# Kernel tuning notes

Hardware: AMD Instinct MI355X
Metric: run time of the kernel (lower is better)

The kernel has to match this reference:

```python
import jax, jax.numpy as jnp
import numpy as np

IOU_TH = 0.5      # iou_threshold
SCORE_TH = 0.5    # confidence_threshold (passed as score_threshold to tf NMS)
MAX_DET = 512     # max_detections


def setup_inputs() -> dict:
    key = jax.random.key(0)
    k1, k2, k3 = jax.random.split(key, 3)
    B, N, C = 8, 2048, 80
    # tf.image.non_max_suppression interprets box columns as corners
    # (y1, x1, y2, x2); generate valid corner boxes in [0, 1].
    mins = jax.random.uniform(k1, (B, N, 2), dtype=jnp.float32)
    sizes = jax.random.uniform(k2, (B, N, 2), dtype=jnp.float32) * 0.2 + 0.01
    box_prediction = jnp.concatenate([mins, mins + sizes], axis=-1)  # [B,N,4]
    class_prediction = jax.random.normal(k3, (B, N, C), dtype=jnp.float32) * 2.0
    return {"box_prediction": box_prediction, "class_prediction": class_prediction}


def _nms_single(boxes, cls_pred, conf):
    """Greedy NMS for one image. boxes [N,4], cls_pred [N,C], conf [N].
    Matches tf.image.non_max_suppression semantics (corner-coordinate IoU,
    score threshold, greedy suppression in descending score order),
    then gathers boxes/cls/conf at the kept indices, padded to MAX_DET."""
    N = boxes.shape[0]
    order = jnp.argsort(-conf)                 # descending scores
    b = boxes[order]                            # [N,4]
    c = cls_pred[order]                         # [N,C]
    s = conf[order]                             # [N]

    bb = jax.lax.stop_gradient(b)               # IoU/indices are non-diff
    y1, x1, y2, x2 = bb[:, 0], bb[:, 1], bb[:, 2], bb[:, 3]
    area = (y2 - y1) * (x2 - x1)                # [N]
    ih = jnp.clip(jnp.minimum(y2[:, None], y2[None, :]) -
                  jnp.maximum(y1[:, None], y1[None, :]), 0.0)
    iw = jnp.clip(jnp.minimum(x2[:, None], x2[None, :]) -
                  jnp.maximum(x1[:, None], x1[None, :]), 0.0)
    inter = ih * iw                             # [N,N]
    union = area[:, None] + area[None, :] - inter
    iou = inter / jnp.maximum(union, 1e-9)      # [N,N]

    valid = s > SCORE_TH                        # score_threshold filter
    idxs = jnp.arange(N)

    def step(keep, xs):
        row, i = xs
        # if box i survives, suppress all later boxes overlapping > IOU_TH
        sup = (row > IOU_TH) & (idxs > i) & keep[i]
        return keep & ~sup, None

    keep, _ = jax.lax.scan(step, valid, (iou, idxs))

    # select kept boxes (already sorted by score) padded to MAX_DET
    masked = jnp.where(keep, s, -1.0)
    top_s, top_idx = jax.lax.top_k(jax.lax.stop_gradient(masked), MAX_DET)
    vm = top_s > SCORE_TH                       # validity of each output slot
    out_box = b[top_idx] * vm[:, None].astype(b.dtype)
    out_cls = c[top_idx] * vm[:, None].astype(c.dtype)
    out_conf = jnp.where(vm, s[top_idx], 0.0)
    return out_box, out_cls, out_conf


def reference(box_prediction, class_prediction):
    # from_logits=True branch of the layer
    class_confidence = jnp.max(jax.nn.sigmoid(class_prediction), axis=-1)  # [B,N]
    cls_prob = jax.nn.softmax(class_prediction, axis=-1)                   # [B,N,C]
    nms_box, nms_cls, nms_conf = jax.vmap(_nms_single)(
        box_prediction, cls_prob, class_confidence)
    return nms_box, nms_cls, nms_conf
```

## Files before the change

### kernel.cpp

```cpp
#include <hip/hip_runtime.h>
#include <stdint.h>

#define BB 8
#define NN 2048
#define NC 80
#define MAXDET 512
#define WPR 32


#define ORD_HALF 0xBF000000u

__global__ void k_conf(const float* __restrict__ cls, uint64_t* __restrict__ keys) {
    int gid = blockIdx.x * blockDim.x + threadIdx.x;
    const float4* p = (const float4*)(cls + (size_t)gid * NC);
    float m = -3.0e38f;
#pragma unroll
    for (int i = 0; i < NC / 4; ++i) {
        float4 v = p[i];
        m = fmaxf(m, fmaxf(fmaxf(v.x, v.y), fmaxf(v.z, v.w)));
    }
    float e  = expf(-m);
    float cf = 1.0f / (1.0f + e);
    uint32_t u = __float_as_uint(cf);
    u = (u & 0x80000000u) ? ~u : (u | 0x80000000u);
    int n = gid & (NN - 1);
    keys[gid] = ((uint64_t)u << 32) | (uint32_t)(NN - 1 - n);
}

#define RCHUNK 128
__global__ __launch_bounds__(512) void k_rank(const uint64_t* __restrict__ keys_in,
                                              uint64_t* __restrict__ keys_out,
                                              const float* __restrict__ boxes,
                                              float* __restrict__ sboxes) {
    __shared__ uint64_t sk[NN];
    __shared__ uint16_t part[4][RCHUNK];
    int b = blockIdx.y, t = threadIdx.x;
    const uint64_t* kin = keys_in + (size_t)b * NN;
#pragma unroll
    for (int j = 0; j < NN / 512; ++j)
        sk[t + j * 512] = kin[t + j * 512];
    __syncthreads();
    int sub = t >> 7;
    int el  = t & (RCHUNK - 1);
    int e   = blockIdx.x * RCHUNK + el;
    uint64_t mykey = sk[e];
    int base = sub * (NN / 4);
    int r = 0;
    for (int mm = 0; mm < NN / 4; ++mm)
        r += (sk[base + mm] > mykey) ? 1 : 0;
    part[sub][el] = (uint16_t)r;
    __syncthreads();
    if (t < RCHUNK) {
        int rank = part[0][t] + part[1][t] + part[2][t] + part[3][t];
        keys_out[(size_t)b * NN + rank] = mykey;
        int orig = (NN - 1) - (int)(mykey & 0xFFFFFFFFull);
        ((float4*)sboxes)[(size_t)b * NN + rank] =
            ((const float4*)boxes)[(size_t)b * NN + orig];
    }
}

__global__ void k_sup(const float* __restrict__ sboxes, uint64_t* __restrict__ sup) {
#pragma clang fp contract(off)
    __shared__ float cy1[256], cx1[256], cy2[256], cx2[256], car[256];
    __shared__ float ry1[64], rx1[64], ry2[64], rx2[64], rar[64];
    int rt = blockIdx.x, ct = blockIdx.y, b = blockIdx.z;
    int t = threadIdx.x;
    int col0 = ct << 8, row0 = rt << 6;
    {
        float4 bx = ((const float4*)sboxes)[(size_t)b * NN + col0 + t];
        cy1[t] = bx.x; cx1[t] = bx.y; cy2[t] = bx.z; cx2[t] = bx.w;
        car[t] = (bx.z - bx.x) * (bx.w - bx.y);
        if (t < 64) {
            float4 rb = ((const float4*)sboxes)[(size_t)b * NN + row0 + t];
            ry1[t] = rb.x; rx1[t] = rb.y; ry2[t] = rb.z; rx2[t] = rb.w;
            rar[t] = (rb.z - rb.x) * (rb.w - rb.y);
        }
    }
    __syncthreads();
    int lr = t & 63, lg = t >> 6;
    int r = row0 + lr;
    int gw = (ct << 2) + lg;
    int cbase = gw << 6;
    uint64_t w = 0;
    if (cbase + 63 > r) {
        float y1 = ry1[lr], x1 = rx1[lr], y2 = ry2[lr], x2 = rx2[lr], ar = rar[lr];
        int lcb = lg << 6;
        for (int c = 0; c < 64; ++c) {
            int lc = lcb + c;
            float ih = fmaxf(fminf(y2, cy2[lc]) - fmaxf(y1, cy1[lc]), 0.0f);
            float iw = fmaxf(fminf(x2, cx2[lc]) - fmaxf(x1, cx1[lc]), 0.0f);
            float inter = ih * iw;
            float uni = (ar + car[lc]) - inter;
            float iou = inter / fmaxf(uni, 1e-9f);
            if ((iou > 0.5f) & ((cbase + c) > r)) w |= (1ull << c);
        }
    }
    sup[((size_t)b * NN + r) * WPR + gw] = w;
}

#define NMS_THREADS 320
__global__ __launch_bounds__(NMS_THREADS) void k_nms(const uint64_t* __restrict__ keys,
                                                     const float* __restrict__ sboxes,
                                                     const uint64_t* __restrict__ sup,
                                                     int* __restrict__ kidx,
                                                     int* __restrict__ kcount,
                                                     float* __restrict__ out_box,
                                                     float* __restrict__ out_conf) {
    __shared__ uint64_t buf[2][64 * WPR];
    __shared__ uint8_t  val[NN];
    __shared__ uint64_t kmaskS[WPR];
    __shared__ int pfx[WPR];
    __shared__ int s_kc;
    __shared__ int s_done;
    int b = blockIdx.x, t = threadIdx.x;
    const uint64_t* supb = sup + (size_t)b * NN * WPR;
    const uint64_t* keyb = keys + (size_t)b * NN;

    for (int i = t; i < NN; i += NMS_THREADS)
        val[i] = (uint8_t)((uint32_t)(keyb[i] >> 32) > ORD_HALF);
    if (t < WPR) kmaskS[t] = 0;
    if (t == 0) s_done = 0;
    for (int w = t; w < 64 * WPR / 2; w += NMS_THREADS)
        ((float4*)buf[0])[w] = ((const float4*)supb)[w];
    __syncthreads();

    int wave = t >> 6;
    uint64_t kb = 0;
    int cnt = 0;
    if (t < 32) {
        uint64_t vm = 0;
#pragma unroll
        for (int c = 0; c < 64; ++c)
            vm |= ((uint64_t)val[(t << 6) | c]) << c;
        kb = ~vm;
    }
    int l2 = t & 31, half = (t >> 5) & 1;

    for (int g = 0; g < WPR; ++g) {
        if (wave > 0) {
            if (g + 1 < WPR) {
                const float4* src = (const float4*)(supb + (size_t)(g + 1) * 64 * WPR);
                float4* dst = (float4*)buf[(g + 1) & 1];
                int idx = t - 64;
                float4 r0 = src[idx];
                float4 r1 = src[idx + 256];
                float4 r2 = src[idx + 512];
                float4 r3 = src[idx + 768];
                dst[idx]       = r0;
                dst[idx + 256] = r1;
                dst[idx + 512] = r2;
                dst[idx + 768] = r3;
            }
        } else {
            const uint64_t* bufc = buf[g & 1];
            uint64_t diag = bufc[t * WPR + g];
            uint32_t dlo = (uint32_t)diag, dhi = (uint32_t)(diag >> 32);
            uint64_t rwv = __shfl(kb, g);
            uint32_t rw_lo = __builtin_amdgcn_readfirstlane((uint32_t)rwv);
            uint32_t rw_hi = __builtin_amdgcn_readfirstlane((uint32_t)(rwv >> 32));
            uint32_t gm_lo = 0, gm_hi = 0;
#pragma unroll
            for (int c = 0; c < 32; ++c) {
                uint32_t rlo = __builtin_amdgcn_readlane(dlo, c);
                uint32_t rhi = __builtin_amdgcn_readlane(dhi, c);
                if (((rw_lo >> c) & 1u) == 0u) {
                    rw_lo |= rlo; rw_hi |= rhi; gm_lo |= (1u << c);
                }
            }
#pragma unroll
            for (int c = 0; c < 32; ++c) {
                uint32_t rlo = __builtin_amdgcn_readlane(dlo, c + 32);
                uint32_t rhi = __builtin_amdgcn_readlane(dhi, c + 32);
                if (((rw_hi >> c) & 1u) == 0u) {
                    rw_lo |= rlo; rw_hi |= rhi; gm_hi |= (1u << c);
                }
            }
            uint64_t gm = ((uint64_t)gm_hi << 32) | gm_lo;
            uint32_t gmh = half ? gm_hi : gm_lo;
            const uint64_t* rowp = bufc + ((half << 5) * WPR + l2);
            uint64_t acc = 0;
#pragma unroll
            for (int j = 0; j < 32; ++j) {
                uint64_t row = rowp[(size_t)j * WPR];
                if ((gmh >> j) & 1u) acc |= row;
            }
            acc |= __shfl(acc, t ^ 32);
            if (t < 32) kb |= acc;
            if (t == g) kmaskS[g] = gm;
            cnt += __popcll(gm);
            if (cnt >= MAXDET) s_done = 1;
        }
        __syncthreads();
        if (s_done) break;
    }

    if (t == 0) {
        int s = 0;
        for (int w2 = 0; w2 < WPR; ++w2) { pfx[w2] = s; s += __popcll(kmaskS[w2]); }
        s_kc = (s < MAXDET) ? s : MAXDET;
        kcount[b] = s_kc;
    }
    __syncthreads();
    for (int i = t; i < NN; i += NMS_THREADS) {
        uint64_t m = kmaskS[i >> 6];
        if ((m >> (i & 63)) & 1ull) {
            int rank = pfx[i >> 6] + __popcll(m & ((1ull << (i & 63)) - 1ull));
            if (rank < MAXDET) {
                ((float4*)out_box)[(size_t)b * MAXDET + rank] =
                    ((const float4*)sboxes)[(size_t)b * NN + i];
                uint64_t kk = keyb[i];
                uint32_t u = (uint32_t)(kk >> 32);
                float cf = (u & 0x80000000u) ? __uint_as_float(u ^ 0x80000000u)
                                             : __uint_as_float(~u);
                out_conf[(size_t)b * MAXDET + rank] = cf;
                kidx[b * MAXDET + rank] = (NN - 1) - (int)(kk & 0xFFFFFFFFull);
            }
        }
    }
    for (int k = s_kc + t; k < MAXDET; k += NMS_THREADS) {
        ((float4*)out_box)[(size_t)b * MAXDET + k] = make_float4(0.f, 0.f, 0.f, 0.f);
        out_conf[(size_t)b * MAXDET + k] = 0.0f;
    }
}

__global__ void k_softmax(const float* __restrict__ cls, const int* __restrict__ kidx,
                          const int* __restrict__ kcount, float* __restrict__ out_cls) {
    int k = blockIdx.x, b = blockIdx.y, lane = threadIdx.x;
    float* dst = out_cls + ((size_t)b * MAXDET + k) * NC;
    if (k >= kcount[b]) {
        dst[lane] = 0.0f;
        if (lane < NC - 64) dst[64 + lane] = 0.0f;
        return;
    }
    int n = kidx[b * MAXDET + k];
    const float* src = cls + ((size_t)b * NN + n) * NC;
    float x0 = src[lane];
    float x1 = (lane < NC - 64) ? src[64 + lane] : -3.0e38f;
    float m = fmaxf(x0, x1);
    for (int o = 32; o > 0; o >>= 1) m = fmaxf(m, __shfl_xor(m, o));
    float e0 = expf(x0 - m);
    float e1 = (lane < NC - 64) ? expf(x1 - m) : 0.0f;
    float s = e0 + e1;
    for (int o = 32; o > 0; o >>= 1) s += __shfl_xor(s, o);
    dst[lane] = e0 / s;
    if (lane < NC - 64) dst[64 + lane] = e1 / s;
}

extern "C" void kernel_launch(void* const* d_in, const int* in_sizes, int n_in,
                              void* d_out, int out_size, void* d_ws, size_t ws_size,
                              hipStream_t stream) {
    const float* boxes = (const float*)d_in[0];
    const float* cls   = (const float*)d_in[1];
    float* out      = (float*)d_out;
    float* out_box  = out;
    float* out_cls  = out + BB * MAXDET * 4;
    float* out_conf = out + BB * MAXDET * (4 + NC);

    char* ws = (char*)d_ws;
    uint64_t* keysA  = (uint64_t*)(ws + 0);
    uint64_t* keysB  = (uint64_t*)(ws + 131072);
    float*    sboxes = (float*)(ws + 262144);
    int*      kidx   = (int*)(ws + 524288);
    int*      kcount = (int*)(ws + 540672);
    uint64_t* sup    = (uint64_t*)(ws + 544768);

    k_conf<<<(BB * NN) / 256, 256, 0, stream>>>(cls, keysA);
    k_rank<<<dim3(NN / RCHUNK, BB), 512, 0, stream>>>(keysA, keysB, boxes, sboxes);
    k_sup<<<dim3(NN / 64, NN / 256, BB), 256, 0, stream>>>(sboxes, sup);
    k_nms<<<BB, NMS_THREADS, 0, stream>>>(keysB, sboxes, sup, kidx, kcount, out_box, out_conf);
    k_softmax<<<dim3(MAXDET, BB), 64, 0, stream>>>(cls, kidx, kcount, out_cls);
}
```

Before: 85.56 us.

## Run NMS sweep in a single wave with direct global row loads

The NMS kernel shrinks from five waves (one compute wave plus four prefetch waves using double-buffered LDS and a block barrier per group) to a single 64-thread wave. That wave loads its 32 suppression rows straight from global memory into registers and exits early without a barrier. The suppression kernel now also writes each row's diagonal word to a compact buffer, so the NMS wave can stage diagonals in LDS up front. The validity mask is built with ballots, and k_conf uses 64-thread blocks. This removes per-step __syncthreads and the LDS copy traffic, but exposes global load latency on the serial critical path.

```diff
diff --git a/kernel.cpp b/kernel.cpp
--- a/kernel.cpp
+++ b/kernel.cpp
@@ -10,8 +10,9 @@
 
 #define ORD_HALF 0xBF000000u
 
-__global__ void k_conf(const float* __restrict__ cls, uint64_t* __restrict__ keys) {
-    int gid = blockIdx.x * blockDim.x + threadIdx.x;
+__global__ __launch_bounds__(64) void k_conf(const float* __restrict__ cls,
+                                             uint64_t* __restrict__ keys) {
+    int gid = blockIdx.x * 64 + threadIdx.x;
     const float4* p = (const float4*)(cls + (size_t)gid * NC);
     float m = -3.0e38f;
 #pragma unroll
@@ -59,7 +60,8 @@
     }
 }
 
-__global__ void k_sup(const float* __restrict__ sboxes, uint64_t* __restrict__ sup) {
+__global__ void k_sup(const float* __restrict__ sboxes, uint64_t* __restrict__ sup,
+                      uint64_t* __restrict__ diagw) {
 #pragma clang fp contract(off)
     __shared__ float cy1[256], cx1[256], cy2[256], cx2[256], car[256];
     __shared__ float ry1[64], rx1[64], ry2[64], rx2[64], rar[64];
@@ -96,103 +98,79 @@
         }
     }
     sup[((size_t)b * NN + r) * WPR + gw] = w;
-}
-
-#define NMS_THREADS 320
-__global__ __launch_bounds__(NMS_THREADS) void k_nms(const uint64_t* __restrict__ keys,
-                                                     const float* __restrict__ sboxes,
-                                                     const uint64_t* __restrict__ sup,
-                                                     int* __restrict__ kidx,
-                                                     int* __restrict__ kcount,
-                                                     float* __restrict__ out_box,
-                                                     float* __restrict__ out_conf) {
-    __shared__ uint64_t buf[2][64 * WPR];
-    __shared__ uint8_t  val[NN];
+    if (gw == (r >> 6)) diagw[(size_t)b * NN + r] = w;
+}
+
+__global__ __launch_bounds__(64) void k_nms(const uint64_t* __restrict__ keys,
+                                            const float* __restrict__ sboxes,
+                                            const uint64_t* __restrict__ sup,
+                                            const uint64_t* __restrict__ diagw,
+                                            int* __restrict__ kidx,
+                                            int* __restrict__ kcount,
+                                            float* __restrict__ out_box,
+                                            float* __restrict__ out_conf) {
+    __shared__ uint64_t dg[NN];
     __shared__ uint64_t kmaskS[WPR];
     __shared__ int pfx[WPR];
     __shared__ int s_kc;
-    __shared__ int s_done;
     int b = blockIdx.x, t = threadIdx.x;
     const uint64_t* supb = sup + (size_t)b * NN * WPR;
     const uint64_t* keyb = keys + (size_t)b * NN;
-
-    for (int i = t; i < NN; i += NMS_THREADS)
-        val[i] = (uint8_t)((uint32_t)(keyb[i] >> 32) > ORD_HALF);
+    const uint64_t* dgb  = diagw + (size_t)b * NN;
+
+    for (int i = t; i < NN; i += 64) dg[i] = dgb[i];
     if (t < WPR) kmaskS[t] = 0;
-    if (t == 0) s_done = 0;
-    for (int w = t; w < 64 * WPR / 2; w += NMS_THREADS)
-        ((float4*)buf[0])[w] = ((const float4*)supb)[w];
-    __syncthreads();
-
-    int wave = t >> 6;
+
     uint64_t kb = 0;
+    for (int i = 0; i < WPR; ++i) {
+        uint32_t hi = (uint32_t)(keyb[(i << 6) + t] >> 32);
+        uint64_t bal = __ballot(hi > ORD_HALF);
+        if (t == i) kb = ~bal;
+    }
+    __syncthreads();
+
+    int l2 = t & 31, half = t >> 5;
     int cnt = 0;
-    if (t < 32) {
-        uint64_t vm = 0;
-#pragma unroll
-        for (int c = 0; c < 64; ++c)
-            vm |= ((uint64_t)val[(t << 6) | c]) << c;
-        kb = ~vm;
-    }
-    int l2 = t & 31, half = (t >> 5) & 1;
-
     for (int g = 0; g < WPR; ++g) {
-        if (wave > 0) {
-            if (g + 1 < WPR) {
-                const float4* src = (const float4*)(supb + (size_t)(g + 1) * 64 * WPR);
-                float4* dst = (float4*)buf[(g + 1) & 1];
-                int idx = t - 64;
-                float4 r0 = src[idx];
-                float4 r1 = src[idx + 256];
-                float4 r2 = src[idx + 512];
-                float4 r3 = src[idx + 768];
-                dst[idx]       = r0;
-                dst[idx + 256] = r1;
-                dst[idx + 512] = r2;
-                dst[idx + 768] = r3;
+        uint64_t diag = dg[(g << 6) + t];
+        uint32_t dlo = (uint32_t)diag, dhi = (uint32_t)(diag >> 32);
+        const uint64_t* rowp = supb + ((size_t)((g << 6) + (half << 5)) * WPR) + l2;
+        uint64_t rows[32];
+#pragma unroll
+        for (int j = 0; j < 32; ++j) rows[j] = rowp[(size_t)j * WPR];
+        uint64_t rwv = __shfl(kb, g);
+        uint32_t rw_lo = __builtin_amdgcn_readfirstlane((uint32_t)rwv);
+        uint32_t rw_hi = __builtin_amdgcn_readfirstlane((uint32_t)(rwv >> 32));
+        uint32_t gm_lo = 0, gm_hi = 0;
+#pragma unroll
+        for (int c = 0; c < 32; ++c) {
+            uint32_t rlo = __builtin_amdgcn_readlane(dlo, c);
+            uint32_t rhi = __builtin_amdgcn_readlane(dhi, c);
+            if (((rw_lo >> c) & 1u) == 0u) {
+                rw_lo |= rlo; rw_hi |= rhi; gm_lo |= (1u << c);
             }
-        } else {
-            const uint64_t* bufc = buf[g & 1];
-            uint64_t diag = bufc[t * WPR + g];
-            uint32_t dlo = (uint32_t)diag, dhi = (uint32_t)(diag >> 32);
-            uint64_t rwv = __shfl(kb, g);
-            uint32_t rw_lo = __builtin_amdgcn_readfirstlane((uint32_t)rwv);
-            uint32_t rw_hi = __builtin_amdgcn_readfirstlane((uint32_t)(rwv >> 32));
-            uint32_t gm_lo = 0, gm_hi = 0;
-#pragma unroll
-            for (int c = 0; c < 32; ++c) {
-                uint32_t rlo = __builtin_amdgcn_readlane(dlo, c);
-                uint32_t rhi = __builtin_amdgcn_readlane(dhi, c);
-                if (((rw_lo >> c) & 1u) == 0u) {
-                    rw_lo |= rlo; rw_hi |= rhi; gm_lo |= (1u << c);
-                }
+        }
+#pragma unroll
+        for (int c = 0; c < 32; ++c) {
+            uint32_t rlo = __builtin_amdgcn_readlane(dlo, c + 32);
+            uint32_t rhi = __builtin_amdgcn_readlane(dhi, c + 32);
+            if (((rw_hi >> c) & 1u) == 0u) {
+                rw_lo |= rlo; rw_hi |= rhi; gm_hi |= (1u << c);
             }
-#pragma unroll
-            for (int c = 0; c < 32; ++c) {
-                uint32_t rlo = __builtin_amdgcn_readlane(dlo, c + 32);
-                uint32_t rhi = __builtin_amdgcn_readlane(dhi, c + 32);
-                if (((rw_hi >> c) & 1u) == 0u) {
-                    rw_lo |= rlo; rw_hi |= rhi; gm_hi |= (1u << c);
-                }
-            }
-            uint64_t gm = ((uint64_t)gm_hi << 32) | gm_lo;
-            uint32_t gmh = half ? gm_hi : gm_lo;
-            const uint64_t* rowp = bufc + ((half << 5) * WPR + l2);
-            uint64_t acc = 0;
-#pragma unroll
-            for (int j = 0; j < 32; ++j) {
-                uint64_t row = rowp[(size_t)j * WPR];
-                if ((gmh >> j) & 1u) acc |= row;
-            }
-            acc |= __shfl(acc, t ^ 32);
-            if (t < 32) kb |= acc;
-            if (t == g) kmaskS[g] = gm;
-            cnt += __popcll(gm);
-            if (cnt >= MAXDET) s_done = 1;
-        }
-        __syncthreads();
-        if (s_done) break;
-    }
+        }
+        uint64_t gm = ((uint64_t)gm_hi << 32) | gm_lo;
+        uint32_t gmh = half ? gm_hi : gm_lo;
+        uint64_t acc = 0;
+#pragma unroll
+        for (int j = 0; j < 32; ++j)
+            acc |= (((gmh >> j) & 1u) ? rows[j] : 0ull);
+        acc |= __shfl(acc, t ^ 32);
+        if (t < 32) kb |= acc;
+        if (t == 0) kmaskS[g] = gm;
+        cnt += __popcll(gm);
+        if (cnt >= MAXDET) break;
+    }
+    __syncthreads();
 
     if (t == 0) {
         int s = 0;
@@ -201,7 +179,7 @@
         kcount[b] = s_kc;
     }
     __syncthreads();
-    for (int i = t; i < NN; i += NMS_THREADS) {
+    for (int i = t; i < NN; i += 64) {
         uint64_t m = kmaskS[i >> 6];
         if ((m >> (i & 63)) & 1ull) {
             int rank = pfx[i >> 6] + __popcll(m & ((1ull << (i & 63)) - 1ull));
@@ -217,7 +195,7 @@
             }
         }
     }
-    for (int k = s_kc + t; k < MAXDET; k += NMS_THREADS) {
+    for (int k = s_kc + t; k < MAXDET; k += 64) {
         ((float4*)out_box)[(size_t)b * MAXDET + k] = make_float4(0.f, 0.f, 0.f, 0.f);
         out_conf[(size_t)b * MAXDET + k] = 0.0f;
     }
@@ -262,11 +240,12 @@
     float*    sboxes = (float*)(ws + 262144);
     int*      kidx   = (int*)(ws + 524288);
     int*      kcount = (int*)(ws + 540672);
-    uint64_t* sup    = (uint64_t*)(ws + 544768);
-
-    k_conf<<<(BB * NN) / 256, 256, 0, stream>>>(cls, keysA);
+    uint64_t* diagw  = (uint64_t*)(ws + 540800);
+    uint64_t* sup    = (uint64_t*)(ws + 671872);
+
+    k_conf<<<(BB * NN) / 64, 64, 0, stream>>>(cls, keysA);
     k_rank<<<dim3(NN / RCHUNK, BB), 512, 0, stream>>>(keysA, keysB, boxes, sboxes);
-    k_sup<<<dim3(NN / 64, NN / 256, BB), 256, 0, stream>>>(sboxes, sup);
-    k_nms<<<BB, NMS_THREADS, 0, stream>>>(keysB, sboxes, sup, kidx, kcount, out_box, out_conf);
+    k_sup<<<dim3(NN / 64, NN / 256, BB), 256, 0, stream>>>(sboxes, sup, diagw);
+    k_nms<<<BB, 64, 0, stream>>>(keysB, sboxes, sup, diagw, kidx, kcount, out_box, out_conf);
     k_softmax<<<dim3(MAXDET, BB), 64, 0, stream>>>(cls, kidx, kcount, out_cls);
 }
```

Result: no change. 86.29 us (+0.9%).
